# Optimization experiments

Hardware: AMD Instinct MI355X
Metric: run time of the kernel (lower is better)

The kernel has to match this reference:

```python
import jax, jax.numpy as jnp
import numpy as np

D = 64            # number of devices (leaves hold D/8 each)
B = 65536         # batch of states
FEAT = 5 + 4 * D  # 261
HID = 128


def setup_inputs() -> dict:
    key = jax.random.key(0)
    ks = jax.random.split(key, 10)
    def nrm(k, shape, s=0.1):
        return jax.random.normal(k, shape, jnp.float32) * s
    return {
        "x": jax.random.normal(ks[0], (B, FEAT), jnp.float32),
        # gate params per depth d: 2^d nodes, weight dim 5 + 4*D/2^d
        "w0": nrm(ks[1], (1, 5 + 4 * D)),
        "b0": jnp.zeros((1,), jnp.float32),
        "w1": nrm(ks[2], (2, 5 + 4 * (D // 2))),
        "b1": jnp.zeros((2,), jnp.float32),
        "w2": nrm(ks[3], (4, 5 + 4 * (D // 4))),
        "b2": jnp.zeros((4,), jnp.float32),
        # leaf prob_dist (torch inits to zeros; random here for a non-trivial baseline)
        "leaf_probs": nrm(ks[4], (8, D // 8), 1.0),
        # critic MLP
        "Wc1": nrm(ks[5], (FEAT, HID)),
        "bc1": jnp.zeros((HID,), jnp.float32),
        "Wc2": nrm(ks[6], (HID, 1)),
        "bc2": jnp.zeros((1,), jnp.float32),
    }


def reference(x, w0, b0, w1, b1, w2, b2, leaf_probs, Wc1, bc1, Wc2, bc2):
    # Batched deterministic ClusterTree routing (exploration disabled).
    x5 = x[:, :5]                       # (B, 5) global features
    dev = x[:, 5:].reshape(B, D, 4)     # (B, D, 4) per-device features
    node = jnp.zeros((B,), jnp.int32)   # current node index at each depth
    cum = jnp.ones((B,), x.dtype)       # product of gate values along path
    for d, (wd, bd) in enumerate([(w0, b0), (w1, b1), (w2, b2)]):
        nd = D >> d                     # devices per node at this depth
        off = node * nd                 # contiguous-cluster start offset
        idx = off[:, None] + jnp.arange(nd)                     # (B, nd)
        dslice = jnp.take_along_axis(dev, idx[:, :, None], 1)   # (B, nd, 4)
        w = wd[node]                    # (B, 5 + 4*nd)
        gate = (jnp.sum(x5 * w[:, :5], -1)
                + jnp.sum(dslice.reshape(B, -1) * w[:, 5:], -1)
                + bd[node])
        val = jax.nn.sigmoid(gate)
        cum = cum * val                 # torch: val * child_output, recursively
        node = node * 2 + (val >= 0.5).astype(jnp.int32)
    p = cum[:, None] * leaf_probs[node]                 # (B, D//8)
    v = jax.nn.relu(x @ Wc1 + bc1) @ Wc2 + bc2          # (B, 1) critic
    return p, v
```

## Files before the change

### kernel.cpp

```cpp
#include <hip/hip_runtime.h>
#include <hip/hip_bf16.h>
#include <stdint.h>

#define NB    65536
#define FEATN 261
#define HIDN  128
#define NSTEP 17
#define SROW  296

#define ROWSG 128
#define NTHRG 512

typedef __attribute__((ext_vector_type(8)))  short bf16x8;
typedef __attribute__((ext_vector_type(16))) float f32x16;
typedef float f32x4u __attribute__((ext_vector_type(4), aligned(4)));

#define MFMA32(A, B, C) __builtin_amdgcn_mfma_f32_32x32x16_bf16(A, B, C, 0, 0, 0)

__device__ __forceinline__ uint16_t f2b(float v) {
    __hip_bfloat16 b = __float2bfloat16(v);
    return *reinterpret_cast<uint16_t*>(&b);
}

__global__ void tree_kernel(
    const float* __restrict__ x,
    const float* __restrict__ w0, const float* __restrict__ b0,
    const float* __restrict__ w1, const float* __restrict__ b1,
    const float* __restrict__ w2, const float* __restrict__ b2,
    const float* __restrict__ leaf,
    const float* __restrict__ Wc1, uint16_t* __restrict__ wsB,
    float* __restrict__ out_p)
{
    const int tid = threadIdx.x;

    if (blockIdx.x < 17) {
        int t = blockIdx.x * 256 + tid;
        if (t < NSTEP * 4 * 64) {
            int p = t >> 6, l = t & 63;
            int s = p >> 2, nt = p & 3;
            int n = nt * 32 + (l & 31);
            int kb = 16 * s + 8 * (l >> 5);
            uint16_t hw[8];
            #pragma unroll
            for (int j = 0; j < 8; ++j) {
                int k = kb + j;
                float v = (k < FEATN) ? Wc1[(size_t)k * HIDN + n] : 0.f;
                hw[j] = f2b(v);
            }
            *reinterpret_cast<uint4*>(wsB + (size_t)p * 512 + l * 8) =
                *reinterpret_cast<uint4*>(hw);
        }
    }

    const int s   = tid & 15;
    const int row = blockIdx.x * 16 + (tid >> 4);
    const float* xr = x + (size_t)row * FEATN;

    f32x4u w0q[4];
    #pragma unroll
    for (int j = 0; j < 4; ++j)
        w0q[j] = *reinterpret_cast<const f32x4u*>(w0 + 4 * s + 64 * j);
    const float w0t = (s < 5) ? w0[256 + s] : 0.f;

    f32x4u w1aq[2], w1bq[2];
    #pragma unroll
    for (int j = 0; j < 2; ++j) {
        w1aq[j] = *reinterpret_cast<const f32x4u*>(w1 + 5 + 8 * s + 4 * j);
        w1bq[j] = *reinterpret_cast<const f32x4u*>(w1 + 133 + 5 + 8 * s + 4 * j);
    }
    const float w1a5 = (s < 5) ? w1[s]       : 0.f;
    const float w1b5 = (s < 5) ? w1[133 + s] : 0.f;

    f32x4u w2q0 = *reinterpret_cast<const f32x4u*>(w2 +  0 * 69 + 5 + 4 * s);
    f32x4u w2q1 = *reinterpret_cast<const f32x4u*>(w2 +  1 * 69 + 5 + 4 * s);
    f32x4u w2q2 = *reinterpret_cast<const f32x4u*>(w2 +  2 * 69 + 5 + 4 * s);
    f32x4u w2q3 = *reinterpret_cast<const f32x4u*>(w2 +  3 * 69 + 5 + 4 * s);
    float w25_0 = (s < 5) ? w2[0 * 69 + s] : 0.f;
    float w25_1 = (s < 5) ? w2[1 * 69 + s] : 0.f;
    float w25_2 = (s < 5) ? w2[2 * 69 + s] : 0.f;
    float w25_3 = (s < 5) ? w2[3 * 69 + s] : 0.f;

    f32x4u xq[4];
    #pragma unroll
    for (int j = 0; j < 4; ++j)
        xq[j] = *reinterpret_cast<const f32x4u*>(xr + 4 * s + 64 * j);
    const float xt  = (s < 5) ? xr[256 + s] : 0.f;
    const float xs5 = (s < 5) ? xr[s]       : 0.f;

    float part = xt * w0t;
    #pragma unroll
    for (int j = 0; j < 4; ++j)
        #pragma unroll
        for (int c = 0; c < 4; ++c)
            part += xq[j][c] * w0q[j][c];
    part += __shfl_xor(part, 1);
    part += __shfl_xor(part, 2);
    part += __shfl_xor(part, 4);
    part += __shfl_xor(part, 8);
    float gate = part + b0[0];
    int node = (gate >= 0.f) ? 1 : 0;
    float cum = 1.f / (1.f + __expf(-gate));

    {
        const float* base = xr + 5 + 128 * node + 8 * s;
        f32x4u xw0 = *reinterpret_cast<const f32x4u*>(base);
        f32x4u xw1 = *reinterpret_cast<const f32x4u*>(base + 4);
        part = xs5 * (node ? w1b5 : w1a5);
        #pragma unroll
        for (int c = 0; c < 4; ++c) {
            part += xw0[c] * (node ? w1bq[0][c] : w1aq[0][c]);
            part += xw1[c] * (node ? w1bq[1][c] : w1aq[1][c]);
        }
        part += __shfl_xor(part, 1);
        part += __shfl_xor(part, 2);
        part += __shfl_xor(part, 4);
        part += __shfl_xor(part, 8);
        gate = part + b1[node];
        cum *= 1.f / (1.f + __expf(-gate));
        node = node * 2 + ((gate >= 0.f) ? 1 : 0);
    }
    {
        f32x4u xv2 = *reinterpret_cast<const f32x4u*>(xr + 5 + 64 * node + 4 * s);
        f32x4u t0 = (node & 1) ? w2q1 : w2q0;
        f32x4u t1 = (node & 1) ? w2q3 : w2q2;
        f32x4u wsel = (node & 2) ? t1 : t0;
        float w5a = (node & 1) ? w25_1 : w25_0;
        float w5b = (node & 1) ? w25_3 : w25_2;
        float w5sel = (node & 2) ? w5b : w5a;
        part = xs5 * w5sel;
        #pragma unroll
        for (int c = 0; c < 4; ++c) part += xv2[c] * wsel[c];
        part += __shfl_xor(part, 1);
        part += __shfl_xor(part, 2);
        part += __shfl_xor(part, 4);
        part += __shfl_xor(part, 8);
        gate = part + b2[node];
        cum *= 1.f / (1.f + __expf(-gate));
        node = node * 2 + ((gate >= 0.f) ? 1 : 0);
    }
    if (s < 8)
        out_p[(size_t)row * 8 + s] = cum * leaf[node * 8 + s];
}

__global__ __launch_bounds__(NTHRG, 2) void critic_gemm(
    const float* __restrict__ x,
    const uint16_t* __restrict__ wsB,
    const float* __restrict__ bc1, const float* __restrict__ Wc2,
    const float* __restrict__ bc2,
    float* __restrict__ out_v)
{
    __shared__ uint16_t Axs[ROWSG * SROW];
    __shared__ float bc1s[HIDN];
    __shared__ float wc2s[HIDN];
    __shared__ float vpart[ROWSG * 2];

    const int tid = threadIdx.x;
    const int rowBase = blockIdx.x * ROWSG;

    if (tid < HIDN) { bc1s[tid] = bc1[tid]; wc2s[tid] = Wc2[tid]; }
    if (tid < ROWSG) {
        uint16_t* rp = Axs + tid * SROW;
        rp[261] = 0;
        *reinterpret_cast<uint32_t*>(rp + 262) = 0u;
        uint4 z; z.x = z.y = z.z = z.w = 0u;
        *reinterpret_cast<uint4*>(rp + 264) = z;
        *reinterpret_cast<uint4*>(rp + 272) = z;
        *reinterpret_cast<uint4*>(rp + 280) = z;
        *reinterpret_cast<uint4*>(rp + 288) = z;
    }

    {
        int row = tid / 66;
        int seg = tid - row * 66;
        #pragma unroll
        for (int it = 0; it < 17; ++it) {
            const int idx = tid + 512 * it;
            if (idx < ROWSG * 66) {
                const float* src = x + (size_t)(rowBase + row) * FEATN + 4 * seg;
                uint16_t* dst = Axs + row * SROW + 4 * seg;
                if (seg < 65) {
                    f32x4u v = *reinterpret_cast<const f32x4u*>(src);
                    uint32_t p0 = (uint32_t)f2b(v[0]) | ((uint32_t)f2b(v[1]) << 16);
                    uint32_t p1 = (uint32_t)f2b(v[2]) | ((uint32_t)f2b(v[3]) << 16);
                    uint2 pk; pk.x = p0; pk.y = p1;
                    *reinterpret_cast<uint2*>(dst) = pk;
                } else {
                    dst[0] = f2b(src[0]);
                }
            }
            row += 7; seg += 50;
            if (seg >= 66) { seg -= 66; row += 1; }
        }
    }
    __syncthreads();

    const int lane = tid & 63;
    const int w    = tid >> 6;
    const int mt   = w >> 1;
    const int nh   = w & 1;

    const uint16_t* arow = Axs + (mt * 32 + (lane & 31)) * SROW + (lane >> 5) * 8;
    const uint16_t* bgl  = wsB + (size_t)(2 * nh) * 512 + lane * 8;

    bf16x8 af[NSTEP], bf0[NSTEP], bf1[NSTEP];
    #pragma unroll
    for (int s = 0; s < NSTEP; ++s) {
        af[s]  = *reinterpret_cast<const bf16x8*>(arow + s * 16);
        bf0[s] = *reinterpret_cast<const bf16x8*>(bgl + (size_t)(s * 4)     * 512);
        bf1[s] = *reinterpret_cast<const bf16x8*>(bgl + (size_t)(s * 4 + 1) * 512);
    }

    f32x16 acc0 = {}, acc1 = {};
    #pragma unroll
    for (int s = 0; s < NSTEP; ++s) {
        acc0 = MFMA32(af[s], bf0[s], acc0);
        acc1 = MFMA32(af[s], bf1[s], acc1);
    }

    {
        const int c = lane & 31;
        const int q = lane >> 5;
        const int n0 = 2 * nh * 32 + c;
        const int n1 = n0 + 32;
        const float bb0 = bc1s[n0], ww0 = wc2s[n0];
        const float bb1 = bc1s[n1], ww1 = wc2s[n1];

        float pv[16];
        #pragma unroll
        for (int reg = 0; reg < 16; ++reg) {
            float h0 = acc0[reg] + bb0; h0 = h0 > 0.f ? h0 : 0.f;
            float h1 = acc1[reg] + bb1; h1 = h1 > 0.f ? h1 : 0.f;
            float t = h0 * ww0 + h1 * ww1;
            t += __shfl_xor(t, 1);
            t += __shfl_xor(t, 2);
            t += __shfl_xor(t, 4);
            t += __shfl_xor(t, 8);
            t += __shfl_xor(t, 16);
            pv[reg] = t;
        }
        #pragma unroll
        for (int reg = 0; reg < 16; ++reg) {
            if (c == reg) {
                int row_local = (reg & 3) + 8 * (reg >> 2) + 4 * q;
                vpart[(mt * 32 + row_local) * 2 + nh] = pv[reg];
            }
        }
    }
    __syncthreads();
    if (tid < ROWSG)
        out_v[rowBase + tid] = vpart[tid * 2] + vpart[tid * 2 + 1] + bc2[0];
}

extern "C" void kernel_launch(void* const* d_in, const int* in_sizes, int n_in,
                              void* d_out, int out_size, void* d_ws, size_t ws_size,
                              hipStream_t stream) {
    const float* x    = (const float*)d_in[0];
    const float* w0   = (const float*)d_in[1];
    const float* b0   = (const float*)d_in[2];
    const float* w1   = (const float*)d_in[3];
    const float* b1   = (const float*)d_in[4];
    const float* w2   = (const float*)d_in[5];
    const float* b2   = (const float*)d_in[6];
    const float* leaf = (const float*)d_in[7];
    const float* Wc1  = (const float*)d_in[8];
    const float* bc1  = (const float*)d_in[9];
    const float* Wc2  = (const float*)d_in[10];
    const float* bc2  = (const float*)d_in[11];

    uint16_t* wsB = (uint16_t*)d_ws;

    float* out_p = (float*)d_out;
    float* out_v = out_p + (size_t)NB * 8;

    tree_kernel<<<NB / 16, 256, 0, stream>>>(
        x, w0, b0, w1, b1, w2, b2, leaf, Wc1, wsB, out_p);
    critic_gemm<<<NB / ROWSG, NTHRG, 0, stream>>>(
        x, wsB, bc1, Wc2, bc2, out_v);
}
```

Before: 138.3 us.

## Merge tree routing and critic GEMM into one kernel with interleaved block roles

Result: slower. 147.4 us (+6.6%).

```diff
diff --git a/kernel.cpp b/kernel.cpp
--- a/kernel.cpp
+++ b/kernel.cpp
@@ -9,7 +9,7 @@
 #define SROW  296
 
 #define ROWSG 128
-#define NTHRG 512
+#define NTHR  512
 
 typedef __attribute__((ext_vector_type(8)))  short bf16x8;
 typedef __attribute__((ext_vector_type(16))) float f32x16;
@@ -22,132 +22,34 @@
     return *reinterpret_cast<uint16_t*>(&b);
 }
 
-__global__ void tree_kernel(
+__global__ void prep_B(const float* __restrict__ Wc1, uint16_t* __restrict__ wsB) {
+    int t = blockIdx.x * blockDim.x + threadIdx.x;
+    if (t >= NSTEP * 4 * 64) return;
+    int p = t >> 6, l = t & 63;
+    int s = p >> 2, nt = p & 3;
+    int n = nt * 32 + (l & 31);
+    int kb = 16 * s + 8 * (l >> 5);
+    uint16_t hw[8];
+    #pragma unroll
+    for (int j = 0; j < 8; ++j) {
+        int k = kb + j;
+        float v = (k < FEATN) ? Wc1[(size_t)k * HIDN + n] : 0.f;
+        hw[j] = f2b(v);
+    }
+    *reinterpret_cast<uint4*>(wsB + (size_t)p * 512 + l * 8) =
+        *reinterpret_cast<uint4*>(hw);
+}
+
+__global__ __launch_bounds__(NTHR) void ac_merged(
     const float* __restrict__ x,
     const float* __restrict__ w0, const float* __restrict__ b0,
     const float* __restrict__ w1, const float* __restrict__ b1,
     const float* __restrict__ w2, const float* __restrict__ b2,
     const float* __restrict__ leaf,
-    const float* __restrict__ Wc1, uint16_t* __restrict__ wsB,
-    float* __restrict__ out_p)
-{
-    const int tid = threadIdx.x;
-
-    if (blockIdx.x < 17) {
-        int t = blockIdx.x * 256 + tid;
-        if (t < NSTEP * 4 * 64) {
-            int p = t >> 6, l = t & 63;
-            int s = p >> 2, nt = p & 3;
-            int n = nt * 32 + (l & 31);
-            int kb = 16 * s + 8 * (l >> 5);
-            uint16_t hw[8];
-            #pragma unroll
-            for (int j = 0; j < 8; ++j) {
-                int k = kb + j;
-                float v = (k < FEATN) ? Wc1[(size_t)k * HIDN + n] : 0.f;
-                hw[j] = f2b(v);
-            }
-            *reinterpret_cast<uint4*>(wsB + (size_t)p * 512 + l * 8) =
-                *reinterpret_cast<uint4*>(hw);
-        }
-    }
-
-    const int s   = tid & 15;
-    const int row = blockIdx.x * 16 + (tid >> 4);
-    const float* xr = x + (size_t)row * FEATN;
-
-    f32x4u w0q[4];
-    #pragma unroll
-    for (int j = 0; j < 4; ++j)
-        w0q[j] = *reinterpret_cast<const f32x4u*>(w0 + 4 * s + 64 * j);
-    const float w0t = (s < 5) ? w0[256 + s] : 0.f;
-
-    f32x4u w1aq[2], w1bq[2];
-    #pragma unroll
-    for (int j = 0; j < 2; ++j) {
-        w1aq[j] = *reinterpret_cast<const f32x4u*>(w1 + 5 + 8 * s + 4 * j);
-        w1bq[j] = *reinterpret_cast<const f32x4u*>(w1 + 133 + 5 + 8 * s + 4 * j);
-    }
-    const float w1a5 = (s < 5) ? w1[s]       : 0.f;
-    const float w1b5 = (s < 5) ? w1[133 + s] : 0.f;
-
-    f32x4u w2q0 = *reinterpret_cast<const f32x4u*>(w2 +  0 * 69 + 5 + 4 * s);
-    f32x4u w2q1 = *reinterpret_cast<const f32x4u*>(w2 +  1 * 69 + 5 + 4 * s);
-    f32x4u w2q2 = *reinterpret_cast<const f32x4u*>(w2 +  2 * 69 + 5 + 4 * s);
-    f32x4u w2q3 = *reinterpret_cast<const f32x4u*>(w2 +  3 * 69 + 5 + 4 * s);
-    float w25_0 = (s < 5) ? w2[0 * 69 + s] : 0.f;
-    float w25_1 = (s < 5) ? w2[1 * 69 + s] : 0.f;
-    float w25_2 = (s < 5) ? w2[2 * 69 + s] : 0.f;
-    float w25_3 = (s < 5) ? w2[3 * 69 + s] : 0.f;
-
-    f32x4u xq[4];
-    #pragma unroll
-    for (int j = 0; j < 4; ++j)
-        xq[j] = *reinterpret_cast<const f32x4u*>(xr + 4 * s + 64 * j);
-    const float xt  = (s < 5) ? xr[256 + s] : 0.f;
-    const float xs5 = (s < 5) ? xr[s]       : 0.f;
-
-    float part = xt * w0t;
-    #pragma unroll
-    for (int j = 0; j < 4; ++j)
-        #pragma unroll
-        for (int c = 0; c < 4; ++c)
-            part += xq[j][c] * w0q[j][c];
-    part += __shfl_xor(part, 1);
-    part += __shfl_xor(part, 2);
-    part += __shfl_xor(part, 4);
-    part += __shfl_xor(part, 8);
-    float gate = part + b0[0];
-    int node = (gate >= 0.f) ? 1 : 0;
-    float cum = 1.f / (1.f + __expf(-gate));
-
-    {
-        const float* base = xr + 5 + 128 * node + 8 * s;
-        f32x4u xw0 = *reinterpret_cast<const f32x4u*>(base);
-        f32x4u xw1 = *reinterpret_cast<const f32x4u*>(base + 4);
-        part = xs5 * (node ? w1b5 : w1a5);
-        #pragma unroll
-        for (int c = 0; c < 4; ++c) {
-            part += xw0[c] * (node ? w1bq[0][c] : w1aq[0][c]);
-            part += xw1[c] * (node ? w1bq[1][c] : w1aq[1][c]);
-        }
-        part += __shfl_xor(part, 1);
-        part += __shfl_xor(part, 2);
-        part += __shfl_xor(part, 4);
-        part += __shfl_xor(part, 8);
-        gate = part + b1[node];
-        cum *= 1.f / (1.f + __expf(-gate));
-        node = node * 2 + ((gate >= 0.f) ? 1 : 0);
-    }
-    {
-        f32x4u xv2 = *reinterpret_cast<const f32x4u*>(xr + 5 + 64 * node + 4 * s);
-        f32x4u t0 = (node & 1) ? w2q1 : w2q0;
-        f32x4u t1 = (node & 1) ? w2q3 : w2q2;
-        f32x4u wsel = (node & 2) ? t1 : t0;
-        float w5a = (node & 1) ? w25_1 : w25_0;
-        float w5b = (node & 1) ? w25_3 : w25_2;
-        float w5sel = (node & 2) ? w5b : w5a;
-        part = xs5 * w5sel;
-        #pragma unroll
-        for (int c = 0; c < 4; ++c) part += xv2[c] * wsel[c];
-        part += __shfl_xor(part, 1);
-        part += __shfl_xor(part, 2);
-        part += __shfl_xor(part, 4);
-        part += __shfl_xor(part, 8);
-        gate = part + b2[node];
-        cum *= 1.f / (1.f + __expf(-gate));
-        node = node * 2 + ((gate >= 0.f) ? 1 : 0);
-    }
-    if (s < 8)
-        out_p[(size_t)row * 8 + s] = cum * leaf[node * 8 + s];
-}
-
-__global__ __launch_bounds__(NTHRG, 2) void critic_gemm(
-    const float* __restrict__ x,
     const uint16_t* __restrict__ wsB,
     const float* __restrict__ bc1, const float* __restrict__ Wc2,
     const float* __restrict__ bc2,
-    float* __restrict__ out_v)
+    float* __restrict__ out_p, float* __restrict__ out_v)
 {
     __shared__ uint16_t Axs[ROWSG * SROW];
     __shared__ float bc1s[HIDN];
@@ -155,100 +57,195 @@
     __shared__ float vpart[ROWSG * 2];
 
     const int tid = threadIdx.x;
-    const int rowBase = blockIdx.x * ROWSG;
-
-    if (tid < HIDN) { bc1s[tid] = bc1[tid]; wc2s[tid] = Wc2[tid]; }
-    if (tid < ROWSG) {
-        uint16_t* rp = Axs + tid * SROW;
-        rp[261] = 0;
-        *reinterpret_cast<uint32_t*>(rp + 262) = 0u;
-        uint4 z; z.x = z.y = z.z = z.w = 0u;
-        *reinterpret_cast<uint4*>(rp + 264) = z;
-        *reinterpret_cast<uint4*>(rp + 272) = z;
-        *reinterpret_cast<uint4*>(rp + 280) = z;
-        *reinterpret_cast<uint4*>(rp + 288) = z;
+    const int g   = blockIdx.x / 5;
+    const int r   = blockIdx.x - 5 * g;
+
+    if (r == 0) {
+        const int rowBase = g * ROWSG;
+
+        if (tid < HIDN) { bc1s[tid] = bc1[tid]; wc2s[tid] = Wc2[tid]; }
+        if (tid < ROWSG) {
+            uint16_t* rp = Axs + tid * SROW;
+            rp[261] = 0;
+            *reinterpret_cast<uint32_t*>(rp + 262) = 0u;
+            uint4 z; z.x = z.y = z.z = z.w = 0u;
+            *reinterpret_cast<uint4*>(rp + 264) = z;
+            *reinterpret_cast<uint4*>(rp + 272) = z;
+            *reinterpret_cast<uint4*>(rp + 280) = z;
+            *reinterpret_cast<uint4*>(rp + 288) = z;
+        }
+
+        {
+            int row = tid / 66;
+            int seg = tid - row * 66;
+            #pragma unroll
+            for (int it = 0; it < 17; ++it) {
+                const int idx = tid + 512 * it;
+                if (idx < ROWSG * 66) {
+                    const float* src = x + (size_t)(rowBase + row) * FEATN + 4 * seg;
+                    uint16_t* dst = Axs + row * SROW + 4 * seg;
+                    if (seg < 65) {
+                        f32x4u v = *reinterpret_cast<const f32x4u*>(src);
+                        uint32_t p0 = (uint32_t)f2b(v[0]) | ((uint32_t)f2b(v[1]) << 16);
+                        uint32_t p1 = (uint32_t)f2b(v[2]) | ((uint32_t)f2b(v[3]) << 16);
+                        uint2 pk; pk.x = p0; pk.y = p1;
+                        *reinterpret_cast<uint2*>(dst) = pk;
+                    } else {
+                        dst[0] = f2b(src[0]);
+                    }
+                }
+                row += 7; seg += 50;
+                if (seg >= 66) { seg -= 66; row += 1; }
+            }
+        }
+        __syncthreads();
+
+        const int lane = tid & 63;
+        const int w    = tid >> 6;
+        const int mt   = w >> 1;
+        const int nh   = w & 1;
+
+        const uint16_t* arow = Axs + (mt * 32 + (lane & 31)) * SROW + (lane >> 5) * 8;
+        const uint16_t* bgl  = wsB + (size_t)(2 * nh) * 512 + lane * 8;
+
+        bf16x8 af[NSTEP], bf0[NSTEP], bf1[NSTEP];
+        #pragma unroll
+        for (int s = 0; s < NSTEP; ++s) {
+            af[s]  = *reinterpret_cast<const bf16x8*>(arow + s * 16);
+            bf0[s] = *reinterpret_cast<const bf16x8*>(bgl + (size_t)(s * 4)     * 512);
+            bf1[s] = *reinterpret_cast<const bf16x8*>(bgl + (size_t)(s * 4 + 1) * 512);
+        }
+
+        f32x16 acc0 = {}, acc1 = {};
+        #pragma unroll
+        for (int s = 0; s < NSTEP; ++s) {
+            acc0 = MFMA32(af[s], bf0[s], acc0);
+            acc1 = MFMA32(af[s], bf1[s], acc1);
+        }
+
+        {
+            const int c = lane & 31;
+            const int q = lane >> 5;
+            const int n0 = 2 * nh * 32 + c;
+            const int n1 = n0 + 32;
+            const float bb0 = bc1s[n0], ww0 = wc2s[n0];
+            const float bb1 = bc1s[n1], ww1 = wc2s[n1];
+
+            float pv[16];
+            #pragma unroll
+            for (int reg = 0; reg < 16; ++reg) {
+                float h0 = acc0[reg] + bb0; h0 = h0 > 0.f ? h0 : 0.f;
+                float h1 = acc1[reg] + bb1; h1 = h1 > 0.f ? h1 : 0.f;
+                float t = h0 * ww0 + h1 * ww1;
+                t += __shfl_xor(t, 1);
+                t += __shfl_xor(t, 2);
+                t += __shfl_xor(t, 4);
+                t += __shfl_xor(t, 8);
+                t += __shfl_xor(t, 16);
+                pv[reg] = t;
+            }
+            #pragma unroll
+            for (int reg = 0; reg < 16; ++reg) {
+                if (c == reg) {
+                    int row_local = (reg & 3) + 8 * (reg >> 2) + 4 * q;
+                    vpart[(mt * 32 + row_local) * 2 + nh] = pv[reg];
+                }
+            }
+        }
+        __syncthreads();
+        if (tid < ROWSG)
+            out_v[rowBase + tid] = vpart[tid * 2] + vpart[tid * 2 + 1] + bc2[0];
+
+    } else {
+        const int s   = tid & 15;
+        const int row = g * ROWSG + (r - 1) * 32 + (tid >> 4);
+        const float* xr = x + (size_t)row * FEATN;
+
+        f32x4u w0q[4];
+        #pragma unroll
+        for (int j = 0; j < 4; ++j)
+            w0q[j] = *reinterpret_cast<const f32x4u*>(w0 + 4 * s + 64 * j);
+        const float w0t = (s < 5) ? w0[256 + s] : 0.f;
+
+        f32x4u w1aq[2], w1bq[2];
+        #pragma unroll
+        for (int j = 0; j < 2; ++j) {
+            w1aq[j] = *reinterpret_cast<const f32x4u*>(w1 + 5 + 8 * s + 4 * j);
+            w1bq[j] = *reinterpret_cast<const f32x4u*>(w1 + 133 + 5 + 8 * s + 4 * j);
+        }
+        const float w1a5 = (s < 5) ? w1[s]       : 0.f;
+        const float w1b5 = (s < 5) ? w1[133 + s] : 0.f;
+
+        f32x4u w2q0 = *reinterpret_cast<const f32x4u*>(w2 + 0 * 69 + 5 + 4 * s);
+        f32x4u w2q1 = *reinterpret_cast<const f32x4u*>(w2 + 1 * 69 + 5 + 4 * s);
+        f32x4u w2q2 = *reinterpret_cast<const f32x4u*>(w2 + 2 * 69 + 5 + 4 * s);
+        f32x4u w2q3 = *reinterpret_cast<const f32x4u*>(w2 + 3 * 69 + 5 + 4 * s);
+        float w25_0 = (s < 5) ? w2[0 * 69 + s] : 0.f;
+        float w25_1 = (s < 5) ? w2[1 * 69 + s] : 0.f;
+        float w25_2 = (s < 5) ? w2[2 * 69 + s] : 0.f;
+        float w25_3 = (s < 5) ? w2[3 * 69 + s] : 0.f;
+
+        f32x4u xq[4];
+        #pragma unroll
+        for (int j = 0; j < 4; ++j)
+            xq[j] = *reinterpret_cast<const f32x4u*>(xr + 4 * s + 64 * j);
+        const float xt  = (s < 5) ? xr[256 + s] : 0.f;
+        const float xs5 = (s < 5) ? xr[s]       : 0.f;
+
+        float part = xt * w0t;
+        #pragma unroll
+        for (int j = 0; j < 4; ++j)
+            #pragma unroll
+            for (int c = 0; c < 4; ++c)
+                part += xq[j][c] * w0q[j][c];
+        part += __shfl_xor(part, 1);
+        part += __shfl_xor(part, 2);
+        part += __shfl_xor(part, 4);
+        part += __shfl_xor(part, 8);
+        float gate = part + b0[0];
+        int node = (gate >= 0.f) ? 1 : 0;
+        float cum = 1.f / (1.f + __expf(-gate));
+
+        {
+            const float* base = xr + 5 + 128 * node + 8 * s;
+            f32x4u xw0 = *reinterpret_cast<const f32x4u*>(base);
+            f32x4u xw1 = *reinterpret_cast<const f32x4u*>(base + 4);
+            part = xs5 * (node ? w1b5 : w1a5);
+            #pragma unroll
+            for (int c = 0; c < 4; ++c) {
+                part += xw0[c] * (node ? w1bq[0][c] : w1aq[0][c]);
+                part += xw1[c] * (node ? w1bq[1][c] : w1aq[1][c]);
+            }
+            part += __shfl_xor(part, 1);
+            part += __shfl_xor(part, 2);
+            part += __shfl_xor(part, 4);
+            part += __shfl_xor(part, 8);
+            gate = part + b1[node];
+            cum *= 1.f / (1.f + __expf(-gate));
+            node = node * 2 + ((gate >= 0.f) ? 1 : 0);
+        }
+        {
+            f32x4u xv2 = *reinterpret_cast<const f32x4u*>(xr + 5 + 64 * node + 4 * s);
+            f32x4u t0 = (node & 1) ? w2q1 : w2q0;
+            f32x4u t1 = (node & 1) ? w2q3 : w2q2;
+            f32x4u wsel = (node & 2) ? t1 : t0;
+            float w5a = (node & 1) ? w25_1 : w25_0;
+            float w5b = (node & 1) ? w25_3 : w25_2;
+            float w5sel = (node & 2) ? w5b : w5a;
+            part = xs5 * w5sel;
+            #pragma unroll
+            for (int c = 0; c < 4; ++c) part += xv2[c] * wsel[c];
+            part += __shfl_xor(part, 1);
+            part += __shfl_xor(part, 2);
+            part += __shfl_xor(part, 4);
+            part += __shfl_xor(part, 8);
+            gate = part + b2[node];
+            cum *= 1.f / (1.f + __expf(-gate));
+            node = node * 2 + ((gate >= 0.f) ? 1 : 0);
+        }
+        if (s < 8)
+            out_p[(size_t)row * 8 + s] = cum * leaf[node * 8 + s];
     }
-
-    {
-        int row = tid / 66;
-        int seg = tid - row * 66;
-        #pragma unroll
-        for (int it = 0; it < 17; ++it) {
-            const int idx = tid + 512 * it;
-            if (idx < ROWSG * 66) {
-                const float* src = x + (size_t)(rowBase + row) * FEATN + 4 * seg;
-                uint16_t* dst = Axs + row * SROW + 4 * seg;
-                if (seg < 65) {
-                    f32x4u v = *reinterpret_cast<const f32x4u*>(src);
-                    uint32_t p0 = (uint32_t)f2b(v[0]) | ((uint32_t)f2b(v[1]) << 16);
-                    uint32_t p1 = (uint32_t)f2b(v[2]) | ((uint32_t)f2b(v[3]) << 16);
-                    uint2 pk; pk.x = p0; pk.y = p1;
-                    *reinterpret_cast<uint2*>(dst) = pk;
-                } else {
-                    dst[0] = f2b(src[0]);
-                }
-            }
-            row += 7; seg += 50;
-            if (seg >= 66) { seg -= 66; row += 1; }
-        }
-    }
-    __syncthreads();
-
-    const int lane = tid & 63;
-    const int w    = tid >> 6;
-    const int mt   = w >> 1;
-    const int nh   = w & 1;
-
-    const uint16_t* arow = Axs + (mt * 32 + (lane & 31)) * SROW + (lane >> 5) * 8;
-    const uint16_t* bgl  = wsB + (size_t)(2 * nh) * 512 + lane * 8;
-
-    bf16x8 af[NSTEP], bf0[NSTEP], bf1[NSTEP];
-    #pragma unroll
-    for (int s = 0; s < NSTEP; ++s) {
-        af[s]  = *reinterpret_cast<const bf16x8*>(arow + s * 16);
-        bf0[s] = *reinterpret_cast<const bf16x8*>(bgl + (size_t)(s * 4)     * 512);
-        bf1[s] = *reinterpret_cast<const bf16x8*>(bgl + (size_t)(s * 4 + 1) * 512);
-    }
-
-    f32x16 acc0 = {}, acc1 = {};
-    #pragma unroll
-    for (int s = 0; s < NSTEP; ++s) {
-        acc0 = MFMA32(af[s], bf0[s], acc0);
-        acc1 = MFMA32(af[s], bf1[s], acc1);
-    }
-
-    {
-        const int c = lane & 31;
-        const int q = lane >> 5;
-        const int n0 = 2 * nh * 32 + c;
-        const int n1 = n0 + 32;
-        const float bb0 = bc1s[n0], ww0 = wc2s[n0];
-        const float bb1 = bc1s[n1], ww1 = wc2s[n1];
-
-        float pv[16];
-        #pragma unroll
-        for (int reg = 0; reg < 16; ++reg) {
-            float h0 = acc0[reg] + bb0; h0 = h0 > 0.f ? h0 : 0.f;
-            float h1 = acc1[reg] + bb1; h1 = h1 > 0.f ? h1 : 0.f;
-            float t = h0 * ww0 + h1 * ww1;
-            t += __shfl_xor(t, 1);
-            t += __shfl_xor(t, 2);
-            t += __shfl_xor(t, 4);
-            t += __shfl_xor(t, 8);
-            t += __shfl_xor(t, 16);
-            pv[reg] = t;
-        }
-        #pragma unroll
-        for (int reg = 0; reg < 16; ++reg) {
-            if (c == reg) {
-                int row_local = (reg & 3) + 8 * (reg >> 2) + 4 * q;
-                vpart[(mt * 32 + row_local) * 2 + nh] = pv[reg];
-            }
-        }
-    }
-    __syncthreads();
-    if (tid < ROWSG)
-        out_v[rowBase + tid] = vpart[tid * 2] + vpart[tid * 2 + 1] + bc2[0];
 }
 
 extern "C" void kernel_launch(void* const* d_in, const int* in_sizes, int n_in,
@@ -272,8 +269,7 @@
     float* out_p = (float*)d_out;
     float* out_v = out_p + (size_t)NB * 8;
 
-    tree_kernel<<<NB / 16, 256, 0, stream>>>(
-        x, w0, b0, w1, b1, w2, b2, leaf, Wc1, wsB, out_p);
-    critic_gemm<<<NB / ROWSG, NTHRG, 0, stream>>>(
-        x, wsB, bc1, Wc2, bc2, out_v);
-}
+    prep_B<<<(NSTEP * 4 * 64 + 255) / 256, 256, 0, stream>>>(Wc1, wsB);
+    ac_merged<<<(NB / ROWSG) * 5, NTHR, 0, stream>>>(
+        x, w0, b0, w1, b1, w2, b2, leaf, wsB, bc1, Wc2, bc2, out_p, out_v);
+}
```
